# Kernel tuning notes

Hardware: AMD Instinct MI355X
Metric: run time of the kernel (lower is better)

## Reference

```python
import jax, jax.numpy as jnp
import numpy as np

IMAGE_SIZE = 256
NUM_FACES = 4096
NEAR = 0.1
FAR = 100.0
DRAW_BACKSIDE = False
EPS = 1e-8
CHUNK = 128  # faces processed per scan step (memory/compute tradeoff)


def setup_inputs() -> dict:
    key = jax.random.key(0)
    u = jax.random.uniform(key, (1, NUM_FACES, 3, 3), dtype=jnp.float32)  # fill=rand
    xy = u[..., :2] * 2.0 - 1.0          # screen coords in [-1, 1]
    z = u[..., 2:] * 20.0 + 1.0          # depths in [1, 21], inside (near, far)
    # shrink triangles toward their centroid -> realistic small screen-space triangles
    center = jnp.mean(xy, axis=2, keepdims=True)
    xy = center + (xy - center) * 0.15
    faces = jnp.concatenate([xy, z], axis=-1)  # [B, F, 3, 3]
    return {"faces": faces}


def _rasterize(faces):
    """Z-buffer triangle rasterization. Returns (depth_map, face_index_map).
    Matches the CUDA 'safe' kernel: per pixel, loop faces; point-in-triangle via
    same-sign edge functions; perspective-correct depth 1/zp = sum(w_i / z_i);
    keep the closest face with zp in (near, far); -1 where nothing is drawn.
    Faces are scanned in chunks to avoid materializing [B, F, S, S]."""
    B, F = faces.shape[0], faces.shape[1]
    S = IMAGE_SIZE
    ax = jnp.arange(S, dtype=jnp.float32)
    # pixel centers in normalized coords: p = (2*i + 1 - S) / S
    yp = (2.0 * ax + 1.0 - S) / S
    xp = (2.0 * ax + 1.0 - S) / S
    YP = yp[None, None, :, None]   # [1,1,S,1]
    XP = xp[None, None, None, :]   # [1,1,1,S]

    n_chunks = F // CHUNK
    fc = faces.reshape(B, n_chunks, CHUNK, 3, 3).transpose(1, 0, 2, 3, 4)  # [n,B,C,3,3]
    bases = jnp.arange(n_chunks, dtype=jnp.int32) * CHUNK

    def body(carry, inp):
        best_depth, best_face = carry          # [B,S,S] each
        fchunk, base = inp                     # [B,C,3,3], scalar face offset
        def vtx(k, c):
            return fchunk[:, :, k, c][..., None, None]  # [B,C,1,1]
        x0, y0, z0 = vtx(0, 0), vtx(0, 1), vtx(0, 2)
        x1, y1, z1 = vtx(1, 0), vtx(1, 1), vtx(1, 2)
        x2, y2, z2 = vtx(2, 0), vtx(2, 1), vtx(2, 2)

        # edge functions (unnormalized barycentric weights), [B,C,S,S]
        w0 = (YP - y1) * (x2 - x1) - (XP - x1) * (y2 - y1)
        w1 = (YP - y2) * (x0 - x2) - (XP - x2) * (y0 - y2)
        w2 = (YP - y0) * (x1 - x0) - (XP - x0) * (y1 - y0)
        inside = (w0 * w1 > 0) & (w1 * w2 > 0)  # strictly same sign -> inside

        w_sum = w0 + w1 + w2                    # sign encodes winding order
        facing = jnp.ones_like(inside) if DRAW_BACKSIDE else (w_sum > 0)

        # perspective-correct depth: zp = 1 / sum((w_i / w_sum) / z_i)
        denom = w0 / z0 + w1 / z1 + w2 / z2
        denom = jnp.where(jnp.abs(denom) > EPS, denom, EPS)
        zp = w_sum / denom

        valid = inside & facing & (NEAR < zp) & (zp < FAR)
        depth = jnp.where(valid, zp, FAR)       # [B,C,S,S]

        chunk_depth = jnp.min(depth, axis=1)            # [B,S,S]
        chunk_idx = jnp.argmin(depth, axis=1)
        update = chunk_depth < best_depth               # strict '<' like the CUDA loop
        best_depth = jnp.where(update, chunk_depth, best_depth)
        best_face = jnp.where(update, (base + chunk_idx).astype(jnp.int32), best_face)
        return (best_depth, best_face), None

    init = (jnp.full((B, S, S), FAR, jnp.float32),
            jnp.full((B, S, S), -1, jnp.int32))
    (best_depth, best_face), _ = jax.lax.scan(body, init, (fc, bases))
    return best_depth, best_face


def reference(faces):
    _, face_index_map = _rasterize(faces)
    return face_index_map  # [B, S, S] int32, -1 where no face covers the pixel
```

## Files before the change

### kernel.cpp

```cpp
#include <hip/hip_runtime.h>

#define S 256
#define NF 4096
#define TILE 16
#define NT 1024
#define SLICES 4
#define CAPC 512
#define NEARF 0.1f
#define FARF 100.0f
#define EPSF 1e-8f

__global__ __launch_bounds__(NT, 4) void raster_tile(const float* __restrict__ faces,
                                                     int* __restrict__ out) {
    __shared__ float4 s_cand[CAPC][4];
    __shared__ unsigned long long s_key[NT];
    __shared__ int s_cnt;

    const int tile = blockIdx.x;
    const int tx0 = (tile & (S / TILE - 1)) * TILE;
    const int ty0 = (tile / (S / TILE)) * TILE;

    const int pix = threadIdx.x & 255;
    const int slice = threadIdx.x >> 8;
    const int px = tx0 + (pix & (TILE - 1));
    const int py = ty0 + (pix / TILE);
    const float xp = (2.0f * px + 1.0f - 256.0f) * (1.0f / 256.0f);
    const float yp = (2.0f * py + 1.0f - 256.0f) * (1.0f / 256.0f);

    const float cxlo = (2.0f * tx0 + 1.0f - 256.0f) * (1.0f / 256.0f) - 1e-5f;
    const float cxhi = (2.0f * (tx0 + TILE - 1) + 1.0f - 256.0f) * (1.0f / 256.0f) + 1e-5f;
    const float cylo = (2.0f * ty0 + 1.0f - 256.0f) * (1.0f / 256.0f) - 1e-5f;
    const float cyhi = (2.0f * (ty0 + TILE - 1) + 1.0f - 256.0f) * (1.0f / 256.0f) + 1e-5f;

    float4 A[4], B[4];
    float Cz[4];
#pragma unroll
    for (int i = 0; i < 4; ++i) {
        const float* p = faces + (size_t)(i * NT + threadIdx.x) * 9;
        A[i] = *(const float4*)p;
        B[i] = *(const float4*)(p + 4);
        Cz[i] = p[8];
    }
    if (threadIdx.x == 0) s_cnt = 0;
    __syncthreads();

#pragma unroll
    for (int i = 0; i < 4; ++i) {
        const float x0 = A[i].x, y0 = A[i].y, x1 = A[i].w;
        const float y1 = B[i].x, x2 = B[i].z, y2 = B[i].w;
        const float bxmin = fminf(x0, fminf(x1, x2));
        const float bxmax = fmaxf(x0, fmaxf(x1, x2));
        const float bymin = fminf(y0, fminf(y1, y2));
        const float bymax = fmaxf(y0, fmaxf(y1, y2));
        bool hit = (bxmax >= cxlo) && (bxmin <= cxhi) &&
                   (bymax >= cylo) && (bymin <= cyhi);
        const float dx21 = __fsub_rn(x2, x1), dy21 = __fsub_rn(y2, y1);
        const float dx02 = __fsub_rn(x0, x2), dy02 = __fsub_rn(y0, y2);
        const float dx10 = __fsub_rn(x1, x0), dy10 = __fsub_rn(y1, y0);
        if (hit) {
            const float a2 = __fsub_rn(__fmul_rn(dx10, dy02 * -1.0f),
                                       __fmul_rn(dx02 * -1.0f, dy10));
            hit = (a2 > -1e-4f);
        }
        if (hit) {
            const int slot = atomicAdd(&s_cnt, 1);
            if (slot < CAPC) {
                s_cand[slot][0] = A[i];
                s_cand[slot][1] = B[i];
                s_cand[slot][2] = make_float4(
                    Cz[i], __int_as_float(i * NT + (int)threadIdx.x), dx21, dy21);
                s_cand[slot][3] = make_float4(dx02, dy02, dx10, dy10);
            }
        }
    }
    __syncthreads();

    float bestd = FARF;
    int bestf = 0x7fffffff;

    const int n = s_cnt;
    if (n <= CAPC) {
        for (int i = slice; i < n; i += SLICES) {
            const float4 a = s_cand[i][0];
            const float4 b = s_cand[i][1];
            const float4 c = s_cand[i][2];
            const float4 d = s_cand[i][3];
            const float X0 = a.x, Y0 = a.y, Z0 = a.z, X1 = a.w;
            const float Y1 = b.x, Z1 = b.y, X2 = b.z, Y2 = b.w;
            const float Z2 = c.x;
            const int f = __float_as_int(c.y);
            const float w0 = __fsub_rn(__fmul_rn(__fsub_rn(yp, Y1), c.z),
                                       __fmul_rn(__fsub_rn(xp, X1), c.w));
            const float w1 = __fsub_rn(__fmul_rn(__fsub_rn(yp, Y2), d.x),
                                       __fmul_rn(__fsub_rn(xp, X2), d.y));
            const float w2 = __fsub_rn(__fmul_rn(__fsub_rn(yp, Y0), d.z),
                                       __fmul_rn(__fsub_rn(xp, X0), d.w));
            const bool inside = (__fmul_rn(w0, w1) > 0.0f) && (__fmul_rn(w1, w2) > 0.0f);
            const float wsum = __fadd_rn(__fadd_rn(w0, w1), w2);
            if (inside && (wsum > 0.0f)) {
                float denom = __fadd_rn(__fadd_rn(__fdiv_rn(w0, Z0), __fdiv_rn(w1, Z1)),
                                        __fdiv_rn(w2, Z2));
                denom = (fabsf(denom) > EPSF) ? denom : EPSF;
                const float zp = __fdiv_rn(wsum, denom);
                if ((zp > NEARF) && (zp < FARF)) {
                    if (zp < bestd || (zp == bestd && f < bestf)) {
                        bestd = zp;
                        bestf = f;
                    }
                }
            }
        }
    } else {
        for (int i = slice; i < NF; i += SLICES) {
            const float* p = faces + (size_t)i * 9;
            const float X0 = p[0], Y0 = p[1], Z0 = p[2];
            const float X1 = p[3], Y1 = p[4], Z1 = p[5];
            const float X2 = p[6], Y2 = p[7], Z2 = p[8];
            const float w0 = __fsub_rn(__fmul_rn(__fsub_rn(yp, Y1), __fsub_rn(X2, X1)),
                                       __fmul_rn(__fsub_rn(xp, X1), __fsub_rn(Y2, Y1)));
            const float w1 = __fsub_rn(__fmul_rn(__fsub_rn(yp, Y2), __fsub_rn(X0, X2)),
                                       __fmul_rn(__fsub_rn(xp, X2), __fsub_rn(Y0, Y2)));
            const float w2 = __fsub_rn(__fmul_rn(__fsub_rn(yp, Y0), __fsub_rn(X1, X0)),
                                       __fmul_rn(__fsub_rn(xp, X0), __fsub_rn(Y1, Y0)));
            const bool inside = (__fmul_rn(w0, w1) > 0.0f) && (__fmul_rn(w1, w2) > 0.0f);
            const float wsum = __fadd_rn(__fadd_rn(w0, w1), w2);
            if (inside && (wsum > 0.0f)) {
                float denom = __fadd_rn(__fadd_rn(__fdiv_rn(w0, Z0), __fdiv_rn(w1, Z1)),
                                        __fdiv_rn(w2, Z2));
                denom = (fabsf(denom) > EPSF) ? denom : EPSF;
                const float zp = __fdiv_rn(wsum, denom);
                if ((zp > NEARF) && (zp < FARF)) {
                    if (zp < bestd || (zp == bestd && i < bestf)) {
                        bestd = zp;
                        bestf = i;
                    }
                }
            }
        }
    }

    s_key[threadIdx.x] =
        ((unsigned long long)__float_as_uint(bestd) << 32) | (unsigned int)bestf;
    __syncthreads();
    if (threadIdx.x < 256) {
        unsigned long long k = s_key[threadIdx.x];
        const unsigned long long k1 = s_key[threadIdx.x + 256];
        const unsigned long long k2 = s_key[threadIdx.x + 512];
        const unsigned long long k3 = s_key[threadIdx.x + 768];
        k = k1 < k ? k1 : k;
        k = k2 < k ? k2 : k;
        k = k3 < k ? k3 : k;
        const float dd = __uint_as_float((unsigned int)(k >> 32));
        const int fi = (int)(unsigned int)k;
        const int opx = tx0 + (threadIdx.x & (TILE - 1));
        const int opy = ty0 + (threadIdx.x / TILE);
        out[opy * S + opx] = (dd < FARF) ? fi : -1;
    }
}

extern "C" void kernel_launch(void* const* d_in, const int* in_sizes, int n_in,
                              void* d_out, int out_size, void* d_ws, size_t ws_size,
                              hipStream_t stream) {
    const float* faces = (const float*)d_in[0];
    int* out = (int*)d_out;
    hipLaunchKernelGGL(raster_tile, dim3((S / TILE) * (S / TILE)), dim3(NT), 0, stream,
                       faces, out);
}
```

Measured before the change: 30.41 us.

## Split each tile into half-tiles and use eight face slices per pixel

Each 16x16 tile is split into two 16x8 half-tiles, doubling the grid to 512 blocks, and each pixel's face loop is now split across 8 slices instead of 4. Face loading is restructured into two groups of two so fewer registers are live at once, and launch bounds are raised to request 8 blocks. The aim is more parallelism on the 256-CU device and a shorter serial candidate loop per thread. In exchange, each face is binned twice, the merge reduction is longer, and the half-tile cull box is tighter.

```diff
diff --git a/kernel.cpp b/kernel.cpp
--- a/kernel.cpp
+++ b/kernel.cpp
@@ -3,73 +3,82 @@
 #define S 256
 #define NF 4096
 #define TILE 16
+#define HTILE 8
 #define NT 1024
-#define SLICES 4
+#define SLICES 8
 #define CAPC 512
 #define NEARF 0.1f
 #define FARF 100.0f
 #define EPSF 1e-8f
 
-__global__ __launch_bounds__(NT, 4) void raster_tile(const float* __restrict__ faces,
+__global__ __launch_bounds__(NT, 8) void raster_tile(const float* __restrict__ faces,
                                                      int* __restrict__ out) {
     __shared__ float4 s_cand[CAPC][4];
     __shared__ unsigned long long s_key[NT];
     __shared__ int s_cnt;
 
-    const int tile = blockIdx.x;
+    const int bx = blockIdx.x;
+    const int tile = bx & 255;
+    const int half = bx >> 8;
     const int tx0 = (tile & (S / TILE - 1)) * TILE;
-    const int ty0 = (tile / (S / TILE)) * TILE;
+    const int ty0 = (tile / (S / TILE)) * TILE + half * HTILE;
 
-    const int pix = threadIdx.x & 255;
-    const int slice = threadIdx.x >> 8;
+    const int pix = threadIdx.x & 127;
+    const int slice = threadIdx.x >> 7;
     const int px = tx0 + (pix & (TILE - 1));
-    const int py = ty0 + (pix / TILE);
+    const int py = ty0 + (pix >> 4);
     const float xp = (2.0f * px + 1.0f - 256.0f) * (1.0f / 256.0f);
     const float yp = (2.0f * py + 1.0f - 256.0f) * (1.0f / 256.0f);
 
     const float cxlo = (2.0f * tx0 + 1.0f - 256.0f) * (1.0f / 256.0f) - 1e-5f;
     const float cxhi = (2.0f * (tx0 + TILE - 1) + 1.0f - 256.0f) * (1.0f / 256.0f) + 1e-5f;
     const float cylo = (2.0f * ty0 + 1.0f - 256.0f) * (1.0f / 256.0f) - 1e-5f;
-    const float cyhi = (2.0f * (ty0 + TILE - 1) + 1.0f - 256.0f) * (1.0f / 256.0f) + 1e-5f;
+    const float cyhi = (2.0f * (ty0 + HTILE - 1) + 1.0f - 256.0f) * (1.0f / 256.0f) + 1e-5f;
 
-    float4 A[4], B[4];
-    float Cz[4];
-#pragma unroll
-    for (int i = 0; i < 4; ++i) {
-        const float* p = faces + (size_t)(i * NT + threadIdx.x) * 9;
-        A[i] = *(const float4*)p;
-        B[i] = *(const float4*)(p + 4);
-        Cz[i] = p[8];
-    }
     if (threadIdx.x == 0) s_cnt = 0;
     __syncthreads();
 
 #pragma unroll
-    for (int i = 0; i < 4; ++i) {
-        const float x0 = A[i].x, y0 = A[i].y, x1 = A[i].w;
-        const float y1 = B[i].x, x2 = B[i].z, y2 = B[i].w;
-        const float bxmin = fminf(x0, fminf(x1, x2));
-        const float bxmax = fmaxf(x0, fmaxf(x1, x2));
-        const float bymin = fminf(y0, fminf(y1, y2));
-        const float bymax = fmaxf(y0, fmaxf(y1, y2));
-        bool hit = (bxmax >= cxlo) && (bxmin <= cxhi) &&
-                   (bymax >= cylo) && (bymin <= cyhi);
-        const float dx21 = __fsub_rn(x2, x1), dy21 = __fsub_rn(y2, y1);
-        const float dx02 = __fsub_rn(x0, x2), dy02 = __fsub_rn(y0, y2);
-        const float dx10 = __fsub_rn(x1, x0), dy10 = __fsub_rn(y1, y0);
-        if (hit) {
-            const float a2 = __fsub_rn(__fmul_rn(dx10, dy02 * -1.0f),
-                                       __fmul_rn(dx02 * -1.0f, dy10));
-            hit = (a2 > -1e-4f);
+    for (int g = 0; g < 2; ++g) {
+        float4 A[2], B[2];
+        float Cz[2];
+#pragma unroll
+        for (int i = 0; i < 2; ++i) {
+            const int f = g * 2048 + i * 1024 + (int)threadIdx.x;
+            const float* p = faces + (size_t)f * 9;
+            A[i] = *(const float4*)p;
+            B[i] = *(const float4*)(p + 4);
+            Cz[i] = p[8];
         }
-        if (hit) {
-            const int slot = atomicAdd(&s_cnt, 1);
-            if (slot < CAPC) {
-                s_cand[slot][0] = A[i];
-                s_cand[slot][1] = B[i];
-                s_cand[slot][2] = make_float4(
-                    Cz[i], __int_as_float(i * NT + (int)threadIdx.x), dx21, dy21);
-                s_cand[slot][3] = make_float4(dx02, dy02, dx10, dy10);
+#pragma unroll
+        for (int i = 0; i < 2; ++i) {
+            const float x0 = A[i].x, y0 = A[i].y, x1 = A[i].w;
+            const float y1 = B[i].x, x2 = B[i].z, y2 = B[i].w;
+            const float bxmin = fminf(x0, fminf(x1, x2));
+            const float bxmax = fmaxf(x0, fmaxf(x1, x2));
+            const float bymin = fminf(y0, fminf(y1, y2));
+            const float bymax = fmaxf(y0, fmaxf(y1, y2));
+            bool hit = (bxmax >= cxlo) && (bxmin <= cxhi) &&
+                       (bymax >= cylo) && (bymin <= cyhi);
+            const float dx21 = __fsub_rn(x2, x1), dy21 = __fsub_rn(y2, y1);
+            const float dx02 = __fsub_rn(x0, x2), dy02 = __fsub_rn(y0, y2);
+            const float dx10 = __fsub_rn(x1, x0), dy10 = __fsub_rn(y1, y0);
+            if (hit) {
+                const float a2 = __fsub_rn(
+                    __fmul_rn(__fsub_rn(x1, x0), __fsub_rn(y2, y0)),
+                    __fmul_rn(__fsub_rn(x2, x0), __fsub_rn(y1, y0)));
+                hit = (a2 > -1e-4f);
+            }
+            if (hit) {
+                const int f = g * 2048 + i * 1024 + (int)threadIdx.x;
+                const int slot = atomicAdd(&s_cnt, 1);
+                if (slot < CAPC) {
+                    s_cand[slot][0] = A[i];
+                    s_cand[slot][1] = B[i];
+                    s_cand[slot][2] =
+                        make_float4(Cz[i], __int_as_float(f), dx21, dy21);
+                    s_cand[slot][3] = make_float4(dx02, dy02, dx10, dy10);
+                }
             }
         }
     }
@@ -142,18 +151,17 @@
     s_key[threadIdx.x] =
         ((unsigned long long)__float_as_uint(bestd) << 32) | (unsigned int)bestf;
     __syncthreads();
-    if (threadIdx.x < 256) {
+    if (threadIdx.x < 128) {
         unsigned long long k = s_key[threadIdx.x];
-        const unsigned long long k1 = s_key[threadIdx.x + 256];
-        const unsigned long long k2 = s_key[threadIdx.x + 512];
-        const unsigned long long k3 = s_key[threadIdx.x + 768];
-        k = k1 < k ? k1 : k;
-        k = k2 < k ? k2 : k;
-        k = k3 < k ? k3 : k;
+#pragma unroll
+        for (int s = 1; s < SLICES; ++s) {
+            const unsigned long long ks = s_key[threadIdx.x + 128 * s];
+            k = ks < k ? ks : k;
+        }
         const float dd = __uint_as_float((unsigned int)(k >> 32));
         const int fi = (int)(unsigned int)k;
         const int opx = tx0 + (threadIdx.x & (TILE - 1));
-        const int opy = ty0 + (threadIdx.x / TILE);
+        const int opy = ty0 + (threadIdx.x >> 4);
         out[opy * S + opx] = (dd < FARF) ? fi : -1;
     }
 }
@@ -163,6 +171,6 @@
                               hipStream_t stream) {
     const float* faces = (const float*)d_in[0];
     int* out = (int*)d_out;
-    hipLaunchKernelGGL(raster_tile, dim3((S / TILE) * (S / TILE)), dim3(NT), 0, stream,
-                       faces, out);
+    hipLaunchKernelGGL(raster_tile, dim3(2 * (S / TILE) * (S / TILE)), dim3(NT), 0,
+                       stream, faces, out);
 }
```

Result: faster. 25.87 us (-14.9%).
